# Performance work log

Hardware: AMD Instinct MI355X
Metric: run time of the kernel (lower is better)

Reference implementation:

```python
import jax, jax.numpy as jnp
import numpy as np

K = 10          # neighbors per span
KTOK = 3        # heads used per span
D = 2.0         # token adjacency threshold
GAMMA = 1.0
MAX_WIDTH = 16
CAP = 128       # cap_spans_per_token
B, L, KTOK_TOTAL = 8, 128, 4


def _enumerate_spans(L, max_width):
    ar = np.arange(L)
    l_g, r_g = np.meshgrid(ar, ar, indexing='ij')
    mask = (r_g >= l_g) & (r_g - l_g + 1 <= max_width)
    l_idx = l_g[mask]
    r_idx = r_g[mask]
    S = l_idx.size
    span2id = np.full((L, L), -1, dtype=np.int64)
    span2id[l_idx, r_idx] = np.arange(S)
    return span2id, l_idx, r_idx, S


def _geom_matrix(L, max_width, span2id, l_idx, r_idx):
    # 8-neighborhood (l+/-1, r+/-1) adjacency over span ids, boolean (S,S)
    S = l_idx.size
    off = np.array([[-1, -1], [-1, 0], [-1, 1], [0, -1], [0, 1], [1, -1], [1, 0], [1, 1]])
    nl = l_idx[:, None] + off[None, :, 0]
    nr = r_idx[:, None] + off[None, :, 1]
    valid = (nl >= 0) & (nr >= 0) & (nl <= nr) & (nr < L) & (nr - nl + 1 <= max_width)
    s2 = span2id[np.clip(nl, 0, L - 1), np.clip(nr, 0, L - 1)]
    rows = np.broadcast_to(np.arange(S)[:, None], s2.shape)
    m = valid & (s2 >= 0)
    Geom = np.zeros((S, S), dtype=bool)
    Geom[rows[m], s2[m]] = True
    np.fill_diagonal(Geom, False)
    return Geom


SPAN2ID, L_IDX, R_IDX, S = _enumerate_spans(L, MAX_WIDTH)
GEOM = jnp.asarray(_geom_matrix(L, MAX_WIDTH, SPAN2ID, L_IDX, R_IDX))


def setup_inputs() -> dict:
    key = jax.random.key(0)
    k1, k2, k3 = jax.random.split(key, 3)
    head_indices = jax.random.randint(k1, (B, L, L, KTOK_TOTAL), 0, L)
    head_weights = jax.random.uniform(k2, (B, L, L, KTOK_TOTAL), dtype=jnp.float32)
    dist = jax.random.uniform(k3, (B, L, L), dtype=jnp.float32) * 8.0
    return {"head_indices": head_indices, "head_weights": head_weights, "dist": dist}


def reference(head_indices, head_weights, dist):
    l_idx = jnp.asarray(L_IDX)
    r_idx = jnp.asarray(R_IDX)
    # gather per-span head indices/weights: (B, S, Ktok)
    idx_all = head_indices[:, l_idx, r_idx, :KTOK]
    w_all = head_weights[:, l_idx, r_idx, :KTOK]
    valid1 = idx_all >= 0
    idx_safe = jnp.clip(idx_all, 0, None)
    w_all = w_all * valid1.astype(w_all.dtype)

    # scatter-add token->span dense matrices: (B, S, L)
    b_ix = jnp.arange(B)[:, None, None]
    s_ix = jnp.arange(S)[None, :, None]
    P_w = jnp.zeros((B, S, L), w_all.dtype).at[b_ix, s_ix, idx_safe].add(w_all)
    P_bin = jnp.zeros((B, S, L), jnp.float32).at[b_ix, s_ix, idx_safe].add(valid1.astype(jnp.float32))

    # token adjacency with self loops
    A = jnp.maximum((dist <= D).astype(jnp.float32), jnp.eye(L, dtype=jnp.float32))
    U_mask = jnp.einsum('bsl,blm->bsm', P_bin, A) > 0.0  # (B, S, L) spans hitting token m

    # top-1 head token -> span one-hot, with per-token span cap
    top1 = jnp.clip(idx_all[:, :, 0], 0, L - 1)
    top1_valid = (idx_all[:, :, 0] >= 0).astype(jnp.float32)
    E = jax.nn.one_hot(top1, L, dtype=jnp.float32) * top1_valid[..., None]  # (B, S, L)
    E = jnp.swapaxes(E, 1, 2)  # (B, L, S)
    E = E * (jnp.cumsum(E, axis=2) <= float(CAP)).astype(jnp.float32)

    # candidate matrix M: (B, S, S)
    M = jnp.einsum('bsl,blt->bst', U_mask.astype(jnp.float32), E) > 0.0
    diag = jnp.arange(S)
    M = M.at[:, diag, diag].set(False)
    M = M | GEOM[None]

    # gate scores Gate = P_w @ exp(-gamma*dist) @ P_w^T
    G = jnp.exp(-GAMMA * dist)
    A_pw = jnp.einsum('bsl,blm->bsm', P_w, G)
    Gate = jnp.einsum('bsm,btm->bst', A_pw, P_w)

    Gate_masked = jnp.where(M, Gate, -jnp.inf)
    topk_vals, topk_idx = jax.lax.top_k(Gate_masked, K)  # (B, S, K)
    N_mask = jnp.isfinite(topk_vals)
    N_idx = topk_idx.astype(jnp.int32)

    # self-loop fill for invalid slots
    rows = jnp.broadcast_to(jnp.arange(S, dtype=N_idx.dtype)[None, :, None], (B, S, K))
    N_idx = jnp.where(N_mask, N_idx, rows)
    N_mask = jnp.ones_like(N_mask)
    return N_idx, N_mask
```

## Files before the change

kernel.cpp:

```cpp
#include <hip/hip_runtime.h>
#include <stdint.h>

#define NB 8
#define LL 128
#define NS 1928
#define NK 10
#define WPB 4

__device__ __forceinline__ int span_id(int l, int r) {
    int off = (l <= 112) ? (l << 4) : (NS - (((128 - l) * (129 - l)) >> 1));
    return off + (r - l);
}

__device__ __forceinline__ float npexp_f32(float x) {
    const float magic = 12582912.0f;
    const float log2e = 1.442695040888963f;
    const float c1 = -6.93145752e-1f;
    const float c2 = -1.42860677e-6f;
    float t = __fmul_rn(x, log2e);
    float q = __fsub_rn(__fadd_rn(t, magic), magic);
    float r = __fmaf_rn(q, c1, x);
    r = __fmaf_rn(q, c2, r);
    float num = __fmaf_rn(r, 5.082762527590693718096e-04f, 6.757896990527504603057e-03f);
    num = __fmaf_rn(num, r, 5.114512081637298353406e-02f);
    num = __fmaf_rn(num, r, 2.473615434895520810817e-01f);
    num = __fmaf_rn(num, r, 7.257664613233124478488e-01f);
    num = __fmaf_rn(num, r, 9.999999999980870924916e-01f);
    float den = __fmaf_rn(r, 2.159509375685829852307e-02f, -2.742335390411667452936e-01f);
    den = __fmaf_rn(den, r, 1.0f);
    float p = __fdiv_rn(num, den);
    int qi = (int)q;
    return __fmul_rn(p, __int_as_float((127 + qi) << 23));
}

__device__ __forceinline__ float keyval(unsigned long long k) {
    return __uint_as_float((unsigned)(k >> 32));
}

__device__ __forceinline__ void wfence() {
    __builtin_amdgcn_wave_barrier();
    __threadfence_block();
    __builtin_amdgcn_wave_barrier();
}

__device__ int wave_partition_fast(unsigned long long* a, int* posL, int* posR,
                                   int pl, int pr, int lane) {
    int pm = pl + ((pr - pl) >> 1);
    unsigned long long vl = a[pl], vm = a[pm], vr = a[pr], tt;
    if (keyval(vm) < keyval(vl)) { tt = vm; vm = vl; vl = tt; }
    if (keyval(vr) < keyval(vm)) { tt = vr; vr = vm; vm = tt; }
    if (keyval(vm) < keyval(vl)) { tt = vm; vm = vl; vl = tt; }
    float vp = keyval(vm);
    unsigned long long vq = a[pr - 1];
    if (lane == 0) { a[pl] = vl; a[pr] = vr; a[pm] = vq; a[pr - 1] = vm; }
    wfence();

    unsigned long long lmask = (1ull << lane) - 1ull;
    int baseL = 0, baseR = 0;
    for (int p0 = pl; p0 <= pr; p0 += 64) {
        int pos = p0 + lane;
        bool inr = (pos <= pr);
        float v = inr ? keyval(a[pos]) : 0.0f;
        bool ge = inr && (pos > pl) && (pos < pr) && (v >= vp);
        bool le = inr && (pos <= pr - 2) && (v <= vp);
        unsigned long long bge = __ballot(ge);
        unsigned long long ble = __ballot(le);
        if (ge) posL[baseL + __popcll(bge & lmask)] = pos;
        if (le) posR[baseR + __popcll(ble & lmask)] = pos;
        baseL += __popcll(bge);
        baseR += __popcll(ble);
    }
    wfence();
    int totGE = baseL, totLE = baseR;
    int maxk = (totGE < totLE) ? totGE : totLE;
    int K = 0;
    for (int base = 0;; base += 64) {
        int k = base + lane;
        bool active = (k < maxk);
        int Lk = active ? posL[k] : 0x7fffffff;
        int Rk = active ? posR[totLE - 1 - k] : -1;
        bool sw = active && (Lk < Rk);
        unsigned long long bm = __ballot(sw);
        int nsw = (~bm == 0ull) ? 64 : (__ffsll((long long)~bm) - 1);
        if (sw && (lane < nsw)) {
            unsigned long long tl = a[Lk], tr = a[Rk];
            a[Lk] = tr; a[Rk] = tl;
        }
        K += nsw;
        if (nsw < 64) break;
    }
    wfence();
    int pi = posL[K];
    if (K > 0) { int rp = posR[totLE - K]; if (rp < pi) pi = rp; }
    if (lane == 0) { tt = a[pi]; a[pi] = a[pr - 1]; a[pr - 1] = tt; }
    wfence();
    return pi;
}

__device__ __forceinline__ void lane_sift(unsigned long long* h, int start, int hm) {
    unsigned long long tmp = h[start];
    int i = start, j = start + start;
    while (j <= hm) {
        if (j < hm && keyval(h[j]) < keyval(h[j + 1])) ++j;
        if (keyval(tmp) < keyval(h[j])) { h[i] = h[j]; i = j; j += j; }
        else break;
    }
    h[i] = tmp;
}

__device__ void wave_heap_top(unsigned long long* a, int lo, int hi, int needlo, int lane) {
    unsigned long long* h = a + lo - 1;
    int hm = hi - lo + 1;
    int half = hm >> 1;
    int maxlvl = 0; { int v = half; while (v >>= 1) ++maxlvl; }
    for (int lvl = maxlvl; lvl >= 0; --lvl) {
        int n0 = 1 << lvl;
        int n1 = (n0 << 1) - 1; if (n1 > half) n1 = half;
        for (int nb = n0; nb <= n1; nb += 64) {
            int node = nb + lane;
            if (node <= n1) lane_sift(h, node, hm);
        }
        wfence();
    }
    int E = hi - needlo + 1;
    if (E > hm - 1) E = hm - 1;
    if (lane == 0) {
        int m = hm;
        for (int e = 0; e < E; ++e) {
            unsigned long long tmp = h[m]; h[m] = h[1]; --m;
            int i = 1, j = 2;
            while (j <= m) {
                if (j < m && keyval(h[j]) < keyval(h[j + 1])) ++j;
                if (keyval(tmp) < keyval(h[j])) { h[i] = h[j]; i = j; j += j; }
                else break;
            }
            h[i] = tmp;
        }
    }
    wfence();
}

__device__ void wave_insertion(unsigned long long* a, int lo, int hi, int lane) {
    int len = hi - lo + 1;
    unsigned long long v = (lane < len) ? a[lo + lane] : 0ull;
    float fv = keyval(v);
    int rank = 0;
    for (int j = 0; j < len; ++j) {
        unsigned long long vj = __shfl(v, j, 64);
        float fj = keyval(vj);
        if ((fj < fv) || (fj == fv && j < lane)) ++rank;
    }
    wfence();
    if (lane < len) a[lo + rank] = v;
    wfence();
}

__device__ void wave_np_sort_top(unsigned long long* a, int n, int lane, int* stk,
                                 int* posL, int* posR) {
    int depth = 0; { int v = n; while (v >>= 1) ++depth; }
    depth *= 2;
    const int TOPLO = n - NK;
    int sp = 0;
    int lo = 0, hi = n - 1;
    for (;;) {
        while (hi - lo > 15) {
            if (depth-- < 0) {
                if (hi >= TOPLO) wave_heap_top(a, lo, hi, (lo > TOPLO ? lo : TOPLO), lane);
                goto pop;
            }
            {
                int pi = wave_partition_fast(a, posL, posR, lo, hi, lane);
                if (pi - lo < hi - pi) {
                    if (lane == 0) { stk[sp * 2] = pi + 1; stk[sp * 2 + 1] = hi; }
                    ++sp; hi = pi - 1;
                } else {
                    if (lane == 0) { stk[sp * 2] = lo; stk[sp * 2 + 1] = pi - 1; }
                    ++sp; lo = pi + 1;
                }
                wfence();
            }
        }
        if (hi > lo && hi >= TOPLO) wave_insertion(a, lo, hi, lane);
pop:
        if (sp == 0) break;
        --sp;
        lo = stk[sp * 2]; hi = stk[sp * 2 + 1];
    }
}

__global__ void top1_kernel(const int* __restrict__ hi,
                            unsigned char* __restrict__ top1,
                            unsigned char* __restrict__ flags) {
    int tid = blockIdx.x * blockDim.x + threadIdx.x;
    if (tid >= NB * NS) return;
    int b = tid / NS, t = tid - b * NS;
    int l, r;
    if (t < 1808) { l = t >> 4; r = l + (t & 15); }
    else {
        l = 113;
        while (l < 127 && span_id(l + 1, l + 1) <= t) ++l;
        r = l + (t - span_id(l, l));
    }
    int i0 = hi[((b * LL + l) * LL + r) * 4];
    top1[b * NS + t] = (unsigned char)(i0 & 127);
    flags[b * NS + t] = 0;
}

__global__ void cap_kernel(const unsigned char* __restrict__ top1,
                           unsigned char* __restrict__ flags) {
    int gw = (blockIdx.x * blockDim.x + threadIdx.x) >> 6;
    int lane = threadIdx.x & 63;
    int b = gw >> 7, l = gw & 127;
    const unsigned char* tb = top1 + b * NS;
    unsigned char* fb = flags + b * NS;
    int cnt = 0;
    for (int t0 = 0; t0 < NS; t0 += 64) {
        int t = t0 + lane;
        int tp = (t < NS) ? (int)tb[t] : 255;
        bool match = (tp == l);
        unsigned long long m = __ballot(match);
        if (match) {
            int pre = __popcll(m & ((1ull << lane) - 1ull));
            fb[t] = (cnt + pre + 1 <= 128) ? 1 : 0;
        }
        cnt += __popcll(m);
    }
}

__device__ __forceinline__ void stage_tables(const int* hb, const float* wb,
                                             const unsigned char* fb,
                                             float4* s_pack, uint16_t* s_lrc) {
    for (int j = threadIdx.x; j < LL * 16; j += 256) {
        int l = j >> 4, w = j & 15, r = l + w;
        if (r < LL) {
            int sid = span_id(l, r);
            int4 iv = *(const int4*)(hb + (l * LL + r) * 4);
            float4 wv = *(const float4*)(wb + (l * LL + r) * 4);
            int ia = iv.x, ib = iv.y, ic = iv.z;
            float wa = wv.x, wb2 = wv.y, wc = wv.z;
            int m0, m1 = 255, m2 = 255;
            float W0, W1 = 0.f, W2 = 0.f;
            if (ia == ib && ib == ic) {
                m0 = ia; W0 = __fadd_rn(__fadd_rn(wa, wb2), wc);
            } else if (ia == ib) {
                float W = __fadd_rn(wa, wb2);
                if (ia < ic) { m0 = ia; W0 = W; m1 = ic; W1 = wc; }
                else         { m0 = ic; W0 = wc; m1 = ia; W1 = W; }
            } else if (ia == ic) {
                float W = __fadd_rn(wa, wc);
                if (ia < ib) { m0 = ia; W0 = W; m1 = ib; W1 = wb2; }
                else         { m0 = ib; W0 = wb2; m1 = ia; W1 = W; }
            } else if (ib == ic) {
                float W = __fadd_rn(wb2, wc);
                if (ia < ib) { m0 = ia; W0 = wa; m1 = ib; W1 = W; }
                else         { m0 = ib; W0 = W; m1 = ia; W1 = wa; }
            } else {
                int x0 = ia, x1 = ib, x2 = ic; float y0 = wa, y1 = wb2, y2 = wc;
                if (x0 > x1) { int tx = x0; x0 = x1; x1 = tx; float ty = y0; y0 = y1; y1 = ty; }
                if (x1 > x2) { int tx = x1; x1 = x2; x2 = tx; float ty = y1; y1 = y2; y2 = ty; }
                if (x0 > x1) { int tx = x0; x0 = x1; x1 = tx; float ty = y0; y0 = y1; y1 = ty; }
                m0 = x0; m1 = x1; m2 = x2; W0 = y0; W1 = y1; W2 = y2;
            }
            uint32_t cap = fb[sid] & 1u;
            uint32_t rec = (uint32_t)m0 | ((uint32_t)m1 << 8) | ((uint32_t)m2 << 16)
                         | ((uint32_t)(ia & 127) << 24);
            s_pack[sid] = make_float4(W0, W1, W2, __uint_as_float(rec));
            s_lrc[sid] = (uint16_t)(l | (r << 7) | (cap << 14));
        }
    }
}

__global__ __launch_bounds__(256)
void span_scan_kernel(const int* __restrict__ hi, const float* __restrict__ hw,
                      const float* __restrict__ dist,
                      const unsigned char* __restrict__ capf,
                      unsigned char* __restrict__ rowflag,
                      int* __restrict__ out) {
    __shared__ float4 s_pack[NS];
    __shared__ uint16_t s_lrc[NS];
    __shared__ float s_q[WPB][LL];

    const int b = blockIdx.y;
    stage_tables(hi + b * LL * LL * 4, hw + b * LL * LL * 4, capf + b * NS, s_pack, s_lrc);
    __syncthreads();

    const int wid = threadIdx.x >> 6;
    const int lane = threadIdx.x & 63;
    const int s = blockIdx.x * WPB + wid;

    float4 ps = s_pack[s];
    uint32_t rec = __float_as_uint(ps.w);
    int m0 = rec & 255, m1 = (rec >> 8) & 255, m2 = (rec >> 16) & 255;
    bool e1 = (m1 != 255), e2 = (m2 != 255);
    uint32_t lrc = s_lrc[s];
    int ls = lrc & 127, rs = (lrc >> 7) & 127;

    const float* db = dist + b * LL * LL;
    const float* row0 = db + m0 * LL;
    const float* row1 = db + (e1 ? m1 : 0) * LL;
    const float* row2 = db + (e2 ? m2 : 0) * LL;
    int mA = lane, mB = lane + 64;
    float dA0 = row0[mA], dB0 = row0[mB];
    float dA1 = row1[mA], dB1 = row1[mB];
    float dA2 = row2[mA], dB2 = row2[mB];
    float qA = __fmaf_rn(ps.x, npexp_f32(-dA0), 0.0f);
    qA = __fmaf_rn(ps.y, npexp_f32(-dA1), qA);
    qA = __fmaf_rn(ps.z, npexp_f32(-dA2), qA);
    float qB = __fmaf_rn(ps.x, npexp_f32(-dB0), 0.0f);
    qB = __fmaf_rn(ps.y, npexp_f32(-dB1), qB);
    qB = __fmaf_rn(ps.z, npexp_f32(-dB2), qB);
    bool cA = (dA0 <= 2.0f || mA == m0) ||
              (e1 && (dA1 <= 2.0f || mA == m1)) ||
              (e2 && (dA2 <= 2.0f || mA == m2));
    bool cB = (dB0 <= 2.0f || mB == m0) ||
              (e1 && (dB1 <= 2.0f || mB == m1)) ||
              (e2 && (dB2 <= 2.0f || mB == m2));
    unsigned long long ub0 = __ballot(cA);
    unsigned long long ub1 = __ballot(cB);
    s_q[wid][mA] = qA;
    s_q[wid][mB] = qB;
    const float* q = s_q[wid];

    unsigned v = 0u; int vi = -1; unsigned tau = 0u;

    for (int t0 = 0; t0 < NS; t0 += 64) {
        int t = t0 + lane;
        unsigned key = 0u;
        if (t < NS) {
            float4 pt = s_pack[t];
            uint32_t rt = __float_as_uint(pt.w);
            float g = __fmaf_rn(pt.x, q[rt & 127], 0.0f);
            g = __fmaf_rn(pt.y, q[(rt >> 8) & 127], g);
            g = __fmaf_rn(pt.z, q[(rt >> 16) & 127], g);
            uint32_t lr = s_lrc[t];
            int lt = lr & 127, rt2 = (lr >> 7) & 127;
            int dl = lt - ls; if (dl < 0) dl = -dl;
            int dr = rt2 - rs; if (dr < 0) dr = -dr;
            bool neq = (t != s);
            bool geom = neq && (dl <= 1) && (dr <= 1);
            int ri0 = rt >> 24;
            unsigned long long bits = (ri0 & 64) ? ub1 : ub0;
            bool um = (((bits >> (ri0 & 63)) & 1ull) != 0) && ((lr >> 14) & 1u) && neq;
            if (um || geom) key = __float_as_uint(g);
        }
        unsigned long long bm = __ballot(key > tau);
        while (bm) {
            int ln = __ffsll((long long)bm) - 1;
            bm &= bm - 1;
            unsigned kk = __shfl(key, ln, 64);
            if (kk > tau) {
                int tk = t0 + ln;
                unsigned vprev = __shfl_up(v, 1, 64);
                int iprev = __shfl_up(vi, 1, 64);
                if (lane == 0) vprev = 0xFFFFFFFFu;
                bool keep = (v >= kk);
                bool fp = (vprev < kk);
                v = keep ? v : (fp ? vprev : kk);
                vi = keep ? vi : (fp ? iprev : tk);
                tau = __shfl(v, 10, 64);
            }
        }
    }

    unsigned vn = __shfl_down(v, 1, 64);
    bool tie = (lane < NK) && (v != 0u) && (vn == v);
    bool flag = (__ballot(tie) != 0ull);

    if (lane < NK) {
        int o = (b * NS + s) * NK + lane;
        out[NB * NS * NK + o] = 1;
        if (!flag) out[o] = (vi >= 0) ? vi : s;
    }
    if (lane == 0) rowflag[b * NS + s] = flag ? 1 : 0;
}

__global__ __launch_bounds__(256)
void span_slow_kernel(const int* __restrict__ hi, const float* __restrict__ hw,
                      const float* __restrict__ dist,
                      const unsigned char* __restrict__ capf,
                      const unsigned char* __restrict__ rowflag,
                      int* __restrict__ out) {
    __shared__ int s_nrows;
    __shared__ int s_rows[256];
    __shared__ float4 s_pack[NS];
    __shared__ uint16_t s_lrc[NS];
    __shared__ float s_qq[LL];
    __shared__ unsigned long long s_cov[2];
    __shared__ unsigned long long s_buf[NS];
    __shared__ int s_posL[NS], s_posR[NS];
    __shared__ int s_stk[48];

    const int b = blockIdx.x;
    if (threadIdx.x == 0) s_nrows = 0;
    __syncthreads();
    for (int i = threadIdx.x; i < NS; i += 256) {
        if (rowflag[b * NS + i]) {
            int k = atomicAdd(&s_nrows, 1);
            if (k < 256) s_rows[k] = i;
        }
    }
    __syncthreads();
    int nrows = s_nrows; if (nrows > 256) nrows = 256;
    if (nrows == 0) return;

    stage_tables(hi + b * LL * LL * 4, hw + b * LL * LL * 4, capf + b * NS, s_pack, s_lrc);
    __syncthreads();

    const int wid = threadIdx.x >> 6;
    const int lane = threadIdx.x & 63;
    const float* db = dist + b * LL * LL;

    for (int ri = 0; ri < nrows; ++ri) {
        const int s = s_rows[ri];
        uint32_t lrc = s_lrc[s];
        int ls = lrc & 127, rs = (lrc >> 7) & 127;

        if (wid == 0) {
            float4 ps = s_pack[s];
            uint32_t rec = __float_as_uint(ps.w);
            int m0 = rec & 255, m1 = (rec >> 8) & 255, m2 = (rec >> 16) & 255;
            bool e1 = (m1 != 255), e2 = (m2 != 255);
            const float* row0 = db + m0 * LL;
            const float* row1 = db + (e1 ? m1 : 0) * LL;
            const float* row2 = db + (e2 ? m2 : 0) * LL;
            int mA = lane, mB = lane + 64;
            float dA0 = row0[mA], dB0 = row0[mB];
            float dA1 = row1[mA], dB1 = row1[mB];
            float dA2 = row2[mA], dB2 = row2[mB];
            float qA = __fmaf_rn(ps.x, npexp_f32(-dA0), 0.0f);
            qA = __fmaf_rn(ps.y, npexp_f32(-dA1), qA);
            qA = __fmaf_rn(ps.z, npexp_f32(-dA2), qA);
            float qB = __fmaf_rn(ps.x, npexp_f32(-dB0), 0.0f);
            qB = __fmaf_rn(ps.y, npexp_f32(-dB1), qB);
            qB = __fmaf_rn(ps.z, npexp_f32(-dB2), qB);
            bool cA = (dA0 <= 2.0f || mA == m0) ||
                      (e1 && (dA1 <= 2.0f || mA == m1)) ||
                      (e2 && (dA2 <= 2.0f || mA == m2));
            bool cB = (dB0 <= 2.0f || mB == m0) ||
                      (e1 && (dB1 <= 2.0f || mB == m1)) ||
                      (e2 && (dB2 <= 2.0f || mB == m2));
            unsigned long long u0 = __ballot(cA);
            unsigned long long u1 = __ballot(cB);
            s_qq[mA] = qA;
            s_qq[mB] = qB;
            if (lane == 0) { s_cov[0] = u0; s_cov[1] = u1; }
        }
        __syncthreads();
        unsigned long long ub0 = s_cov[0], ub1 = s_cov[1];

        for (int t = threadIdx.x; t < NS; t += 256) {
            float4 pt = s_pack[t];
            uint32_t rt = __float_as_uint(pt.w);
            float g = __fmaf_rn(pt.x, s_qq[rt & 127], 0.0f);
            g = __fmaf_rn(pt.y, s_qq[(rt >> 8) & 127], g);
            g = __fmaf_rn(pt.z, s_qq[(rt >> 16) & 127], g);
            uint32_t lr = s_lrc[t];
            int lt = lr & 127, rt2 = (lr >> 7) & 127;
            int dl = lt - ls; if (dl < 0) dl = -dl;
            int dr = rt2 - rs; if (dr < 0) dr = -dr;
            bool neq = (t != s);
            bool geom = neq && (dl <= 1) && (dr <= 1);
            int ri0 = rt >> 24;
            unsigned long long bits = (ri0 & 64) ? ub1 : ub0;
            bool um = (((bits >> (ri0 & 63)) & 1ull) != 0) && ((lr >> 14) & 1u) && neq;
            unsigned h32 = (um || geom) ? __float_as_uint(g) : 0xFF800000u;
            s_buf[t] = ((unsigned long long)h32 << 32) | (unsigned)t;
        }
        __syncthreads();

        if (wid == 0) {
            wave_np_sort_top(s_buf, NS, lane, s_stk, s_posL, s_posR);
            if (lane < NK) {
                unsigned long long k = s_buf[NS - 1 - lane];
                int idx = ((unsigned)(k >> 32) == 0xFF800000u) ? s : (int)(k & 0xffffffffull);
                out[(b * NS + s) * NK + lane] = idx;
            }
        }
        __syncthreads();
    }
}

extern "C" void kernel_launch(void* const* d_in, const int* in_sizes, int n_in,
                              void* d_out, int out_size, void* d_ws, size_t ws_size,
                              hipStream_t stream) {
    const int* hi = (const int*)d_in[0];
    const float* hw = (const float*)d_in[1];
    const float* dist = (const float*)d_in[2];
    int* out = (int*)d_out;

    unsigned char* ws = (unsigned char*)d_ws;
    unsigned char* top1 = ws;
    unsigned char* capf = ws + NB * NS;
    unsigned char* rowflag = ws + 2 * NB * NS;

    int n1 = NB * NS;
    top1_kernel<<<(n1 + 255) / 256, 256, 0, stream>>>(hi, top1, capf);
    cap_kernel<<<(NB * LL * 64) / 256, 256, 0, stream>>>(top1, capf);
    dim3 grid(NS / WPB, NB);
    span_scan_kernel<<<grid, 256, 0, stream>>>(hi, hw, dist, capf, rowflag, out);
    span_slow_kernel<<<NB, 256, 0, stream>>>(hi, hw, dist, capf, rowflag, out);
}
```

Baseline: 240.2 us.

## Process four span rows per wavefront to amortize table staging and scan reads

Each wavefront now computes top-k for four consecutive span rows instead of one. Query vectors are interleaved into float4 shared entries, so one scan pass over the span table serves all four rows. The grid shrinks fourfold, which amortizes the per-block shared-table staging and the per-candidate shared-memory loads. In exchange it raises register pressure (four sets of top-k state and masks) and serializes four ballot/insert loops per chunk.

```diff
diff --git a/kernel.cpp b/kernel.cpp
--- a/kernel.cpp
+++ b/kernel.cpp
@@ -6,6 +6,7 @@
 #define NS 1928
 #define NK 10
 #define WPB 4
+#define G 4
 
 __device__ __forceinline__ int span_id(int l, int r) {
     int off = (l <= 112) ? (l << 4) : (NS - (((128 - l) * (129 - l)) >> 1));
@@ -278,7 +279,7 @@
                       int* __restrict__ out) {
     __shared__ float4 s_pack[NS];
     __shared__ uint16_t s_lrc[NS];
-    __shared__ float s_q[WPB][LL];
+    __shared__ float4 s_q4[WPB][LL];
 
     const int b = blockIdx.y;
     stage_tables(hi + b * LL * LL * 4, hw + b * LL * LL * 4, capf + b * NS, s_pack, s_lrc);
@@ -286,92 +287,120 @@
 
     const int wid = threadIdx.x >> 6;
     const int lane = threadIdx.x & 63;
-    const int s = blockIdx.x * WPB + wid;
-
-    float4 ps = s_pack[s];
-    uint32_t rec = __float_as_uint(ps.w);
-    int m0 = rec & 255, m1 = (rec >> 8) & 255, m2 = (rec >> 16) & 255;
-    bool e1 = (m1 != 255), e2 = (m2 != 255);
-    uint32_t lrc = s_lrc[s];
-    int ls = lrc & 127, rs = (lrc >> 7) & 127;
+    const int sb = blockIdx.x * (WPB * G) + wid * G;
+    if (sb >= NS) return;
 
     const float* db = dist + b * LL * LL;
-    const float* row0 = db + m0 * LL;
-    const float* row1 = db + (e1 ? m1 : 0) * LL;
-    const float* row2 = db + (e2 ? m2 : 0) * LL;
-    int mA = lane, mB = lane + 64;
-    float dA0 = row0[mA], dB0 = row0[mB];
-    float dA1 = row1[mA], dB1 = row1[mB];
-    float dA2 = row2[mA], dB2 = row2[mB];
-    float qA = __fmaf_rn(ps.x, npexp_f32(-dA0), 0.0f);
-    qA = __fmaf_rn(ps.y, npexp_f32(-dA1), qA);
-    qA = __fmaf_rn(ps.z, npexp_f32(-dA2), qA);
-    float qB = __fmaf_rn(ps.x, npexp_f32(-dB0), 0.0f);
-    qB = __fmaf_rn(ps.y, npexp_f32(-dB1), qB);
-    qB = __fmaf_rn(ps.z, npexp_f32(-dB2), qB);
-    bool cA = (dA0 <= 2.0f || mA == m0) ||
-              (e1 && (dA1 <= 2.0f || mA == m1)) ||
-              (e2 && (dA2 <= 2.0f || mA == m2));
-    bool cB = (dB0 <= 2.0f || mB == m0) ||
-              (e1 && (dB1 <= 2.0f || mB == m1)) ||
-              (e2 && (dB2 <= 2.0f || mB == m2));
-    unsigned long long ub0 = __ballot(cA);
-    unsigned long long ub1 = __ballot(cB);
-    s_q[wid][mA] = qA;
-    s_q[wid][mB] = qB;
-    const float* q = s_q[wid];
-
-    unsigned v = 0u; int vi = -1; unsigned tau = 0u;
+    const int mA = lane, mB = lane + 64;
+
+    int lsv[G], rsv[G];
+    unsigned long long u0v[G], u1v[G];
+
+#pragma unroll
+    for (int g = 0; g < G; ++g) {
+        int s = sb + g;
+        float4 ps = s_pack[s];
+        uint32_t rec = __float_as_uint(ps.w);
+        int m0 = rec & 255, m1 = (rec >> 8) & 255, m2 = (rec >> 16) & 255;
+        bool e1 = (m1 != 255), e2 = (m2 != 255);
+        uint32_t lrc = s_lrc[s];
+        lsv[g] = lrc & 127; rsv[g] = (lrc >> 7) & 127;
+        const float* row0 = db + m0 * LL;
+        const float* row1 = db + (e1 ? m1 : 0) * LL;
+        const float* row2 = db + (e2 ? m2 : 0) * LL;
+        float dA0 = row0[mA], dB0 = row0[mB];
+        float dA1 = row1[mA], dB1 = row1[mB];
+        float dA2 = row2[mA], dB2 = row2[mB];
+        float qA = __fmaf_rn(ps.x, npexp_f32(-dA0), 0.0f);
+        qA = __fmaf_rn(ps.y, npexp_f32(-dA1), qA);
+        qA = __fmaf_rn(ps.z, npexp_f32(-dA2), qA);
+        float qB = __fmaf_rn(ps.x, npexp_f32(-dB0), 0.0f);
+        qB = __fmaf_rn(ps.y, npexp_f32(-dB1), qB);
+        qB = __fmaf_rn(ps.z, npexp_f32(-dB2), qB);
+        bool cA = (dA0 <= 2.0f || mA == m0) ||
+                  (e1 && (dA1 <= 2.0f || mA == m1)) ||
+                  (e2 && (dA2 <= 2.0f || mA == m2));
+        bool cB = (dB0 <= 2.0f || mB == m0) ||
+                  (e1 && (dB1 <= 2.0f || mB == m1)) ||
+                  (e2 && (dB2 <= 2.0f || mB == m2));
+        u0v[g] = __ballot(cA);
+        u1v[g] = __ballot(cB);
+        ((float*)&s_q4[wid][mA])[g] = qA;
+        ((float*)&s_q4[wid][mB])[g] = qB;
+    }
+    wfence();
+
+    unsigned v[G], tau[G]; int vi[G];
+#pragma unroll
+    for (int g = 0; g < G; ++g) { v[g] = 0u; tau[g] = 0u; vi[g] = -1; }
 
     for (int t0 = 0; t0 < NS; t0 += 64) {
         int t = t0 + lane;
-        unsigned key = 0u;
+        unsigned key[G];
+#pragma unroll
+        for (int g = 0; g < G; ++g) key[g] = 0u;
         if (t < NS) {
             float4 pt = s_pack[t];
             uint32_t rt = __float_as_uint(pt.w);
-            float g = __fmaf_rn(pt.x, q[rt & 127], 0.0f);
-            g = __fmaf_rn(pt.y, q[(rt >> 8) & 127], g);
-            g = __fmaf_rn(pt.z, q[(rt >> 16) & 127], g);
+            float4 qv0 = s_q4[wid][rt & 127];
+            float4 qv1 = s_q4[wid][(rt >> 8) & 127];
+            float4 qv2 = s_q4[wid][(rt >> 16) & 127];
+            float a0[G] = {qv0.x, qv0.y, qv0.z, qv0.w};
+            float a1[G] = {qv1.x, qv1.y, qv1.z, qv1.w};
+            float a2[G] = {qv2.x, qv2.y, qv2.z, qv2.w};
             uint32_t lr = s_lrc[t];
             int lt = lr & 127, rt2 = (lr >> 7) & 127;
-            int dl = lt - ls; if (dl < 0) dl = -dl;
-            int dr = rt2 - rs; if (dr < 0) dr = -dr;
-            bool neq = (t != s);
-            bool geom = neq && (dl <= 1) && (dr <= 1);
             int ri0 = rt >> 24;
-            unsigned long long bits = (ri0 & 64) ? ub1 : ub0;
-            bool um = (((bits >> (ri0 & 63)) & 1ull) != 0) && ((lr >> 14) & 1u) && neq;
-            if (um || geom) key = __float_as_uint(g);
-        }
-        unsigned long long bm = __ballot(key > tau);
-        while (bm) {
-            int ln = __ffsll((long long)bm) - 1;
-            bm &= bm - 1;
-            unsigned kk = __shfl(key, ln, 64);
-            if (kk > tau) {
-                int tk = t0 + ln;
-                unsigned vprev = __shfl_up(v, 1, 64);
-                int iprev = __shfl_up(vi, 1, 64);
-                if (lane == 0) vprev = 0xFFFFFFFFu;
-                bool keep = (v >= kk);
-                bool fp = (vprev < kk);
-                v = keep ? v : (fp ? vprev : kk);
-                vi = keep ? vi : (fp ? iprev : tk);
-                tau = __shfl(v, 10, 64);
-            }
-        }
-    }
-
-    unsigned vn = __shfl_down(v, 1, 64);
-    bool tie = (lane < NK) && (v != 0u) && (vn == v);
-    bool flag = (__ballot(tie) != 0ull);
-
-    if (lane < NK) {
-        int o = (b * NS + s) * NK + lane;
-        out[NB * NS * NK + o] = 1;
-        if (!flag) out[o] = (vi >= 0) ? vi : s;
-    }
-    if (lane == 0) rowflag[b * NS + s] = flag ? 1 : 0;
+            unsigned capb = (lr >> 14) & 1u;
+#pragma unroll
+            for (int g = 0; g < G; ++g) {
+                float gate = __fmaf_rn(pt.x, a0[g], 0.0f);
+                gate = __fmaf_rn(pt.y, a1[g], gate);
+                gate = __fmaf_rn(pt.z, a2[g], gate);
+                int dl = lt - lsv[g]; if (dl < 0) dl = -dl;
+                int dr = rt2 - rsv[g]; if (dr < 0) dr = -dr;
+                bool neq = (t != sb + g);
+                bool geom = neq && (dl <= 1) && (dr <= 1);
+                unsigned long long bits = (ri0 & 64) ? u1v[g] : u0v[g];
+                bool um = (((bits >> (ri0 & 63)) & 1ull) != 0) && capb && neq;
+                if (um || geom) key[g] = __float_as_uint(gate);
+            }
+        }
+#pragma unroll
+        for (int g = 0; g < G; ++g) {
+            unsigned long long bm = __ballot(key[g] > tau[g]);
+            while (bm) {
+                int ln = __ffsll((long long)bm) - 1;
+                bm &= bm - 1;
+                unsigned kk = __shfl(key[g], ln, 64);
+                if (kk > tau[g]) {
+                    int tk = t0 + ln;
+                    unsigned vprev = __shfl_up(v[g], 1, 64);
+                    int iprev = __shfl_up(vi[g], 1, 64);
+                    if (lane == 0) vprev = 0xFFFFFFFFu;
+                    bool keep = (v[g] >= kk);
+                    bool fp = (vprev < kk);
+                    v[g] = keep ? v[g] : (fp ? vprev : kk);
+                    vi[g] = keep ? vi[g] : (fp ? iprev : tk);
+                    tau[g] = __shfl(v[g], 10, 64);
+                }
+            }
+        }
+    }
+
+#pragma unroll
+    for (int g = 0; g < G; ++g) {
+        int s = sb + g;
+        unsigned vn = __shfl_down(v[g], 1, 64);
+        bool tie = (lane < NK) && (v[g] != 0u) && (vn == v[g]);
+        bool flag = (__ballot(tie) != 0ull);
+        if (lane < NK) {
+            int o = (b * NS + s) * NK + lane;
+            out[NB * NS * NK + o] = 1;
+            if (!flag) out[o] = (vi[g] >= 0) ? vi[g] : s;
+        }
+        if (lane == 0) rowflag[b * NS + s] = flag ? 1 : 0;
+    }
 }
 
 __global__ __launch_bounds__(256)
@@ -496,7 +525,7 @@
     int n1 = NB * NS;
     top1_kernel<<<(n1 + 255) / 256, 256, 0, stream>>>(hi, top1, capf);
     cap_kernel<<<(NB * LL * 64) / 256, 256, 0, stream>>>(top1, capf);
-    dim3 grid(NS / WPB, NB);
+    dim3 grid((NS + WPB * G - 1) / (WPB * G), NB);
     span_scan_kernel<<<grid, 256, 0, stream>>>(hi, hw, dist, capf, rowflag, out);
     span_slow_kernel<<<NB, 256, 0, stream>>>(hi, hw, dist, capf, rowflag, out);
 }
```

Measured after the change: 256.4 us. +6.8%, slower.
